# Kernel tuning notes

Hardware: AMD Instinct MI355X
Metric: run time of the kernel (lower is better)

The kernel has to match this reference:

```python
import jax, jax.numpy as jnp
import numpy as np

N = 100_000      # nodes
E = 1_600_000    # edges (avg degree 16)
D_IN = 128
D_OUT = 128
K = 64           # low-rank attention rank


def setup_inputs() -> dict:
    key = jax.random.key(0)
    ks = jax.random.split(key, 6)
    s = lambda d: 1.0 / np.sqrt(d)
    return {
        "x": jax.random.normal(ks[0], (N, D_IN), dtype=jnp.float32),
        "edge_index": jax.random.randint(ks[1], (2, E), 0, N, dtype=jnp.int32),
        "W_gcn": jax.random.normal(ks[2], (D_IN, D_OUT), dtype=jnp.float32) * s(D_IN),
        "b_gcn": jnp.zeros((D_OUT,), jnp.float32),
        "W_att": jax.random.normal(ks[3], (D_IN, 4 * K), dtype=jnp.float32) * s(D_IN),
        "b_att": jnp.zeros((4 * K,), jnp.float32),
        "W_red": jax.random.normal(ks[4], (D_OUT + 2 * K, D_OUT), dtype=jnp.float32) * s(D_OUT + 2 * K),
        "b_red": jnp.zeros((D_OUT,), jnp.float32),
    }


def _forward(x, W_gcn, b_gcn, W_att, b_att, W_red, b_red, edge_index):
    n = x.shape[0]
    # --- GCN conv (symmetric normalization, self-loops), dropout = identity (eval) ---
    loop = jnp.arange(n, dtype=edge_index.dtype)
    src = jnp.concatenate([edge_index[0], loop])
    dst = jnp.concatenate([edge_index[1], loop])
    deg = jax.ops.segment_sum(jnp.ones_like(dst, dtype=x.dtype), dst, num_segments=n)
    dinv = jax.lax.rsqrt(deg)                      # deg >= 1 due to self-loops
    norm = dinv[src] * dinv[dst]                   # [E+n]
    h = x @ W_gcn                                  # [n, D_OUT]
    agg = jax.ops.segment_sum(h[src] * norm[:, None], dst, num_segments=n) + b_gcn
    x_local = jax.nn.relu(agg)

    # --- Low-rank global attention (LRGA) ---
    t = jax.nn.relu(x @ W_att + b_att)             # [n, 4K]
    U, V, Z, T = jnp.split(t, 4, axis=1)           # each [n, K]
    # joint_normalize2: scalar 1/mean(U @ (V^T @ 1_n))
    D = 1.0 / jnp.mean(U @ (V.T @ jnp.ones((n, 1), x.dtype)))
    res = (U @ (V.T @ Z)) * D                      # [n, K]
    x_global = jnp.concatenate([res, T], axis=1)   # [n, 2K]

    # --- fuse + dim reduce ---
    return jnp.concatenate([x_local, x_global], axis=1) @ W_red + b_red


def reference(x, edge_index, W_gcn, b_gcn, W_att, b_att, W_red, b_red):
    return _forward(x, W_gcn, b_gcn, W_att, b_att, W_red, b_red, edge_index)
```

## Files before the change

### kernel.cpp

```cpp
#include <hip/hip_runtime.h>

#define DIN   128
#define DOUT  128
#define KR    64
#define TCOLS 256
#define WCOLS 384
#define P_RED 512
#define PSTR  4224
#define STCAP 6144

typedef unsigned short ushort_t;
typedef __attribute__((ext_vector_type(8))) short bf16x8;
typedef __attribute__((ext_vector_type(4))) float f32x4;

__device__ __forceinline__ float bf2f(unsigned short u) {
  return __uint_as_float(((unsigned int)u) << 16);
}
__device__ __forceinline__ unsigned short f2bf(float f) {
  unsigned int b = __float_as_uint(f);
  b = b + 0x7FFFu + ((b >> 16) & 1u);
  return (unsigned short)(b >> 16);
}

__global__ __launch_bounds__(256) void k_init(int* __restrict__ degc, float* __restrict__ VtZ,
                                              float* __restrict__ colsum, int* __restrict__ bcur,
                                              int* __restrict__ ocnt, int N) {
  int i = blockIdx.x * 256 + threadIdx.x;
  if (i < N) degc[i] = 1;
  if (i < 4096) VtZ[i] = 0.f;
  if (i < 128) colsum[i] = 0.f;
  if (i < 128) bcur[i] = 0;
  if (i == 0) ocnt[0] = 0;
}

__global__ __launch_bounds__(256) void k_split(const float* __restrict__ x,
                                               ushort_t* __restrict__ xhF, ushort_t* __restrict__ xloF,
                                               int N, int total_slots) {
  int gid = blockIdx.x * 256 + threadIdx.x;
  int stride = gridDim.x * 256;
  for (; gid < total_slots; gid += stride) {
    int f = gid >> 6, l = gid & 63;
    int r16 = f >> 2, s = f & 3;
    int row = r16 * 16 + (l & 15);
    int k = s * 32 + ((l >> 4) << 3);
    ushort4 h0, h1, l0, l1;
    if (row < N) {
      float4 a = *(const float4*)&x[(size_t)row * DIN + k];
      float4 b = *(const float4*)&x[(size_t)row * DIN + k + 4];
      h0.x = f2bf(a.x); h0.y = f2bf(a.y); h0.z = f2bf(a.z); h0.w = f2bf(a.w);
      h1.x = f2bf(b.x); h1.y = f2bf(b.y); h1.z = f2bf(b.z); h1.w = f2bf(b.w);
      l0.x = f2bf(a.x - bf2f(h0.x)); l0.y = f2bf(a.y - bf2f(h0.y));
      l0.z = f2bf(a.z - bf2f(h0.z)); l0.w = f2bf(a.w - bf2f(h0.w));
      l1.x = f2bf(b.x - bf2f(h1.x)); l1.y = f2bf(b.y - bf2f(h1.y));
      l1.z = f2bf(b.z - bf2f(h1.z)); l1.w = f2bf(b.w - bf2f(h1.w));
    } else {
      h0 = make_ushort4(0, 0, 0, 0); h1 = h0; l0 = h0; l1 = h0;
    }
    ((ushort4*)xhF)[gid * 2] = h0;
    ((ushort4*)xhF)[gid * 2 + 1] = h1;
    ((ushort4*)xloF)[gid * 2] = l0;
    ((ushort4*)xloF)[gid * 2 + 1] = l1;
  }
}

__global__ __launch_bounds__(256) void k_wprep(const float* __restrict__ Wg, const float* __restrict__ Wa,
                                               ushort_t* __restrict__ whF, ushort_t* __restrict__ wlF) {
  int g = blockIdx.x * 256 + threadIdx.x;
  int f = g >> 6, l = g & 63;
  int c16 = f >> 2, s = f & 3;
  int col = c16 * 16 + (l & 15);
  int k = s * 32 + ((l >> 4) << 3);
#pragma unroll
  for (int j = 0; j < 8; ++j) {
    float v = (col < DOUT) ? Wg[(size_t)(k + j) * DOUT + col]
                           : Wa[(size_t)(k + j) * TCOLS + (col - DOUT)];
    ushort_t h = f2bf(v);
    whF[(size_t)g * 8 + j] = h;
    wlF[(size_t)g * 8 + j] = f2bf(v - bf2f(h));
  }
}

__global__ __launch_bounds__(256) void k_scan1(const int* __restrict__ degc, int* __restrict__ offs,
                                               int* __restrict__ bsums, int N) {
  __shared__ int s[256];
  int tid = threadIdx.x;
  int base = blockIdx.x * 1024 + tid * 4;
  int c[4], e[4];
#pragma unroll
  for (int q = 0; q < 4; ++q) c[q] = (base + q < N) ? (degc[base + q] - 1) : 0;
  e[0] = 0; e[1] = c[0]; e[2] = e[1] + c[1]; e[3] = e[2] + c[2];
  int tsum = e[3] + c[3];
  s[tid] = tsum; __syncthreads();
  for (int off = 1; off < 256; off <<= 1) {
    int v = (tid >= off) ? s[tid - off] : 0;
    __syncthreads();
    s[tid] += v;
    __syncthreads();
  }
  int tb = s[tid] - tsum;
#pragma unroll
  for (int q = 0; q < 4; ++q) if (base + q < N) offs[base + q] = tb + e[q];
  if (tid == 255) bsums[blockIdx.x] = s[255];
}

__global__ __launch_bounds__(128) void k_scan2(const int* __restrict__ bsums, int* __restrict__ boff,
                                               int* __restrict__ offs, int NBLK, int N) {
  __shared__ int s[128];
  int tid = threadIdx.x;
  int v = (tid < NBLK) ? bsums[tid] : 0;
  s[tid] = v; __syncthreads();
  for (int off = 1; off < 128; off <<= 1) {
    int u = (tid >= off) ? s[tid - off] : 0;
    __syncthreads();
    s[tid] += u;
    __syncthreads();
  }
  boff[tid] = s[tid] - v;
  if (tid == 127) offs[N] = s[127];
}

__global__ __launch_bounds__(256) void k_scan3(int* __restrict__ offs, const int* __restrict__ boff,
                                               const int* __restrict__ degc, float* __restrict__ dinv,
                                               int N) {
  int i = blockIdx.x * 256 + threadIdx.x;
  if (i < N) {
    offs[i] += boff[i >> 10];
    dinv[i] = rsqrtf((float)degc[i]);
  }
}

__global__ __launch_bounds__(256) void k_bin(const int* __restrict__ ei, int* __restrict__ bcur,
                                             int* __restrict__ degc,
                                             int2* __restrict__ buckets,
                                             int2* __restrict__ oflow, int* __restrict__ ocnt,
                                             int E, int B, int CAP) {
  __shared__ int hist[128], pref[128], place[128], gbase[128];
  __shared__ int2 st[4096];
  int tid = threadIdx.x;
  int e0 = blockIdx.x * 4096;
  int nE = min(4096, E - e0);
  if (nE <= 0) return;

  if (tid < 128) { hist[tid] = 0; place[tid] = 0; }
  __syncthreads();

  int src[16], dst[16];
#pragma unroll
  for (int q = 0; q < 16; ++q) {
    int idx = tid + q * 256;
    if (idx < nE) {
      src[q] = ei[e0 + idx];
      dst[q] = ei[E + e0 + idx];
      atomicAdd(&hist[dst[q] >> 10], 1);
      atomicAdd(&degc[dst[q]], 1);
    }
  }
  __syncthreads();

  if (tid < 128) pref[tid] = hist[tid];
  __syncthreads();
  for (int off = 1; off < 128; off <<= 1) {
    int v = (tid < 128 && tid >= off) ? pref[tid - off] : 0;
    __syncthreads();
    if (tid < 128) pref[tid] += v;
    __syncthreads();
  }
  if (tid < 128) pref[tid] -= hist[tid];
  if (tid < B && hist[tid] > 0) gbase[tid] = atomicAdd(&bcur[tid], hist[tid]);
  __syncthreads();

#pragma unroll
  for (int q = 0; q < 16; ++q) {
    int idx = tid + q * 256;
    if (idx < nE) {
      int b = dst[q] >> 10;
      int p = pref[b] + atomicAdd(&place[b], 1);
      st[p] = make_int2(src[q], dst[q]);
    }
  }
  __syncthreads();

  for (int i = tid; i < nE; i += 256) {
    int2 q = st[i];
    int b = q.y >> 10;
    int gp = gbase[b] + (i - pref[b]);
    if (gp < CAP) {
      buckets[(size_t)b * CAP + gp] = q;
    } else {
      int oi = atomicAdd(ocnt, 1);
      oflow[oi] = q;
    }
  }
}

__global__ __launch_bounds__(256) void k_scatter2(const int2* __restrict__ buckets,
                                                  const int* __restrict__ bcur,
                                                  const int* __restrict__ offs,
                                                  const float* __restrict__ dinv,
                                                  const int2* __restrict__ oflow,
                                                  const int* __restrict__ ocnt,
                                                  int2* __restrict__ csr, int CAP, int N) {
  __shared__ int lcur[256];
  __shared__ int2 st[STCAP];
  int cb = blockIdx.x >> 2;
  int lo = cb * 1024 + (blockIdx.x & 3) * 256;
  if (lo >= N) return;
  int tid = threadIdx.x;
  int nnode = min(256, N - lo);
  int base = offs[lo];
  int nb = offs[lo + nnode] - base;
  if (tid < nnode) lcur[tid] = offs[lo + tid];
  __syncthreads();
  int avail = min(bcur[cb], CAP);
  const int2* sp = &buckets[(size_t)cb * CAP];
  bool staged = (nb <= STCAP);
  int quarter = lo >> 8;
  for (int i = tid; i < avail; i += 256) {
    int2 q = sp[i];
    if ((q.y >> 8) != quarter) continue;
    int p = atomicAdd(&lcur[q.y - lo], 1);
    int2 c;
    c.x = q.x;
    c.y = __float_as_int(dinv[q.x] * dinv[q.y]);
    if (staged) st[p - base] = c;
    else        csr[p] = c;
  }
  __syncthreads();
  if (staged) {
    for (int i = tid; i < nb; i += 256) csr[base + i] = st[i];
  }
  __syncthreads();
  int n = ocnt[0];
  for (int i = tid; i < n; i += 256) {
    int2 q = oflow[i];
    if ((q.y >> 8) != quarter) continue;
    int p = atomicAdd(&lcur[q.y - lo], 1);
    int2 c;
    c.x = q.x;
    c.y = __float_as_int(dinv[q.x] * dinv[q.y]);
    csr[p] = c;
  }
}

#define LOADK(S, AH, AL, BH, BL)                                              \
  {                                                                           \
    _Pragma("unroll") for (int m_ = 0; m_ < 4; ++m_) {                        \
      size_t fo_ = (((size_t)(r16b + m_) * 4 + (S)) * 64 + lane) * 8;         \
      AH[m_] = *(const bf16x8*)&xhF[fo_];                                     \
      AL[m_] = *(const bf16x8*)&xloF[fo_];                                    \
    }                                                                         \
    _Pragma("unroll") for (int n_ = 0; n_ < 4; ++n_) {                        \
      size_t fo_ = (((size_t)(c16b + n_) * 4 + (S)) * 64 + lane) * 8;         \
      BH[n_] = *(const bf16x8*)&whF[fo_];                                     \
      BL[n_] = *(const bf16x8*)&wlF[fo_];                                     \
    }                                                                         \
  }

__global__ __launch_bounds__(256) void k_gemm1_mfma(const ushort_t* __restrict__ xhF,
                                                    const ushort_t* __restrict__ xloF,
                                                    const ushort_t* __restrict__ whF,
                                                    const ushort_t* __restrict__ wlF,
                                                    const float* __restrict__ ba,
                                                    ushort_t* __restrict__ hs, ushort_t* __restrict__ t,
                                                    int N, int ntiles) {
  int bid = blockIdx.x;
  int g = bid / 24;
  int rem = bid - g * 24;
  int colblk = rem >> 3;
  int ytile = g * 8 + (rem & 7);
  if (ytile >= ntiles) return;

  int tid = threadIdx.x;
  int lane = tid & 63;
  int wave = tid >> 6;
  int wr = wave >> 1, wc = wave & 1;
  int rowbase = ytile * 128 + wr * 64;
  int gcb = colblk * 128 + wc * 64;
  int r16b = ytile * 8 + wr * 4;
  int c16b = colblk * 8 + wc * 4;
  int lr = lane & 15;
  int rq = (lane >> 4) * 4;

  f32x4 acc[4][4] = {};
  bf16x8 ah[2][4], al[2][4], bh[2][4], bl[2][4];

  LOADK(0, ah[0], al[0], bh[0], bl[0]);
#pragma unroll
  for (int s = 0; s < 4; ++s) {
    int cur = s & 1, nxt = cur ^ 1;
    if (s < 3) LOADK(s + 1, ah[nxt], al[nxt], bh[nxt], bl[nxt]);
#pragma unroll
    for (int m = 0; m < 4; ++m)
#pragma unroll
      for (int n = 0; n < 4; ++n) {
        acc[m][n] = __builtin_amdgcn_mfma_f32_16x16x32_bf16(ah[cur][m], bl[cur][n], acc[m][n], 0, 0, 0);
        acc[m][n] = __builtin_amdgcn_mfma_f32_16x16x32_bf16(al[cur][m], bh[cur][n], acc[m][n], 0, 0, 0);
        acc[m][n] = __builtin_amdgcn_mfma_f32_16x16x32_bf16(ah[cur][m], bh[cur][n], acc[m][n], 0, 0, 0);
      }
  }

  if (colblk == 0) {
#pragma unroll
    for (int m = 0; m < 4; ++m)
#pragma unroll
      for (int i = 0; i < 4; ++i) {
        int row = rowbase + m * 16 + rq + i;
        if (row < N) {
#pragma unroll
          for (int n = 0; n < 4; ++n)
            hs[(size_t)row * DOUT + gcb + n * 16 + lr] = f2bf(acc[m][n][i]);
        }
      }
  } else {
    float bav[4];
#pragma unroll
    for (int n = 0; n < 4; ++n) bav[n] = ba[gcb - DOUT + n * 16 + lr];
#pragma unroll
    for (int m = 0; m < 4; ++m)
#pragma unroll
      for (int i = 0; i < 4; ++i) {
        int row = rowbase + m * 16 + rq + i;
        if (row < N) {
#pragma unroll
          for (int n = 0; n < 4; ++n)
            t[(size_t)row * TCOLS + gcb - DOUT + n * 16 + lr] =
                f2bf(fmaxf(acc[m][n][i] + bav[n], 0.f));
        }
      }
  }
}

#define STAGE_RED(BUF, TILE)                                                     \
  {                                                                              \
    int r0_ = (TILE) * 32;                                                       \
    for (int i_ = tid; i_ < 768; i_ += 256) {                                    \
      int r_ = i_ / 24, c0_ = (i_ % 24) * 8;                                     \
      int row_ = r0_ + r_;                                                       \
      ushort4 v0_, v1_;                                                          \
      if (row_ < N) {                                                            \
        v0_ = ((const ushort4*)&t[(size_t)row_ * TCOLS + c0_])[0];               \
        v1_ = ((const ushort4*)&t[(size_t)row_ * TCOLS + c0_])[1];               \
      } else {                                                                   \
        v0_ = make_ushort4(0, 0, 0, 0); v1_ = v0_;                               \
      }                                                                          \
      *(ushort4*)&ts[BUF][r_ * 200 + c0_] = v0_;                                 \
      *(ushort4*)&ts[BUF][r_ * 200 + c0_ + 4] = v1_;                             \
    }                                                                            \
  }

__global__ __launch_bounds__(256) void k_red(const ushort_t* __restrict__ t, float* __restrict__ part,
                                             int N) {
  __shared__ ushort_t ts[2][32 * 200];
  __shared__ float csh[512];
  int tid = threadIdx.x;
  int lane = tid & 63;
  int w = tid >> 6;
  int lr = lane & 15;
  int lk = (lane >> 4) * 8;
  int vcol = 64 + w * 16 + lr;
  int col2 = lane * 2;

  f32x4 acc[4] = {};
  float cs0 = 0.f, cs1 = 0.f;
  int ntiles = (N + 31) >> 5;
  int cur = 0;

  int tile = blockIdx.x;
  if (tile < ntiles) STAGE_RED(0, tile);
  __syncthreads();
  for (; tile < ntiles; tile += gridDim.x) {
    int nxt = tile + gridDim.x;
    if (nxt < ntiles) STAGE_RED(cur ^ 1, nxt);
    const ushort_t* tb = ts[cur];
    bf16x8 a, b[4];
#pragma unroll
    for (int j = 0; j < 8; ++j)
      ((ushort_t*)&a)[j] = tb[(lk + j) * 200 + vcol];
#pragma unroll
    for (int n = 0; n < 4; ++n)
#pragma unroll
      for (int j = 0; j < 8; ++j)
        ((ushort_t*)&b[n])[j] = tb[(lk + j) * 200 + 128 + n * 16 + lr];
#pragma unroll
    for (int j = 0; j < 8; ++j) {
      ushort2 u = *(const ushort2*)&tb[(w * 8 + j) * 200 + col2];
      cs0 += bf2f(u.x); cs1 += bf2f(u.y);
    }
#pragma unroll
    for (int n = 0; n < 4; ++n)
      acc[n] = __builtin_amdgcn_mfma_f32_16x16x32_bf16(a, b[n], acc[n], 0, 0, 0);
    __syncthreads();
    cur ^= 1;
  }

  float* pb = &part[(size_t)blockIdx.x * PSTR];
  int rq = (lane >> 4) * 4;
#pragma unroll
  for (int n = 0; n < 4; ++n)
#pragma unroll
    for (int i = 0; i < 4; ++i)
      pb[(w * 16 + rq + i) * 64 + n * 16 + lr] = acc[n][i];

  csh[tid] = cs0;
  csh[256 + tid] = cs1;
  __syncthreads();
  if (w == 0) {
    float t0 = csh[lane] + csh[64 + lane] + csh[128 + lane] + csh[192 + lane];
    float t1 = csh[256 + lane] + csh[320 + lane] + csh[384 + lane] + csh[448 + lane];
    pb[4096 + col2] = t0;
    pb[4096 + col2 + 1] = t1;
  }
}

__global__ __launch_bounds__(256) void k_redsum(const float* __restrict__ part,
                                                float* __restrict__ VtZ, float* __restrict__ colsum) {
  __shared__ float s[256];
  int tid = threadIdx.x;
  int j = blockIdx.x * 64 + (tid & 63);
  int bc = tid >> 6;
  float a = 0.f;
#pragma unroll 4
  for (int b = bc; b < P_RED; b += 4) a += part[(size_t)b * PSTR + j];
  s[tid] = a;
  __syncthreads();
  if (bc == 0) {
    float v = s[tid] + s[tid + 64] + s[tid + 128] + s[tid + 192];
    if (j < 4096) VtZ[j] = v;
    else colsum[j - 4096] = v;
  }
}

__global__ __launch_bounds__(256) void k_prep(const float* __restrict__ VtZ,
                                              const float* __restrict__ colsum,
                                              const float* __restrict__ Wr,
                                              ushort_t* __restrict__ weffF, int N) {
  __shared__ float dsh[64];
  __shared__ float Dsh;
  int tid = threadIdx.x;
  if (tid < 64) dsh[tid] = colsum[tid] * colsum[64 + tid];
  __syncthreads();
  if (tid == 0) {
    float p = 0.f;
#pragma unroll 8
    for (int i = 0; i < 64; ++i) p += dsh[i];
    Dsh = (p != 0.f) ? ((float)N / p) : 0.f;
  }
  __syncthreads();
  float Dv = Dsh;

  int g = blockIdx.x * 256 + tid;
  int f = g >> 6, l = g & 63;
  int c16 = f >> 3, s = f & 7;
  int c = c16 * 16 + (l & 15);
  int k0 = s * 32 + ((l >> 4) << 3);
#pragma unroll
  for (int j = 0; j < 8; ++j) {
    int k = k0 + j;
    float v;
    if (k < 128 || k >= 192) {
      v = Wr[(size_t)k * DOUT + c];
    } else {
      int kk = k - 128;
      float acc = 0.f;
      for (int q = 0; q < 64; ++q)
        acc += VtZ[kk * 64 + q] * Wr[(size_t)(128 + q) * DOUT + c];
      v = acc * Dv;
    }
    weffF[(size_t)g * 8 + j] = f2bf(v);
  }
}

__global__ __launch_bounds__(256) void k_aggout(const ushort_t* __restrict__ hs,
                                                const int2* __restrict__ csr,
                                                const int* __restrict__ offs,
                                                const float* __restrict__ dinv,
                                                const float* __restrict__ bg,
                                                const ushort_t* __restrict__ t,
                                                const ushort_t* __restrict__ weffF,
                                                const float* __restrict__ br,
                                                float* __restrict__ out, int N) {
  __shared__ ushort_t ys[32 * 264];
  int tid = threadIdx.x;
  int lane = tid & 63;
  int w = tid >> 6;
  int lr = lane & 15;
  int lk = (lane >> 4) * 8;
  int rq = (lane >> 4) * 4;
  int r0 = blockIdx.x * 32;
  int c2 = 2 * lane;

  for (int i = tid; i < 512; i += 256) {
    int r = i >> 4, c0 = 128 + (i & 15) * 8;
    int row = r0 + r;
    ushort4 v0, v1;
    if (row < N) {
      const ushort_t* src = (c0 < 192) ? &t[(size_t)row * TCOLS + (c0 - 128)]
                                       : &t[(size_t)row * TCOLS + c0];
      v0 = ((const ushort4*)src)[0];
      v1 = ((const ushort4*)src)[1];
    } else {
      v0 = make_ushort4(0, 0, 0, 0); v1 = v0;
    }
    *(ushort4*)&ys[r * 264 + c0] = v0;
    *(ushort4*)&ys[r * 264 + c0 + 4] = v1;
  }

  float bg0 = bg[c2], bg1 = bg[c2 + 1];
  for (int q = 0; q < 8; ++q) {
    int r = w * 8 + q;
    int node = r0 + r;
    ushort2 o = make_ushort2(0, 0);
    if (node < N) {
      float dn = dinv[node];
      ushort2 u = *(const ushort2*)&hs[(size_t)node * DOUT + c2];
      float a0 = dn * dn * bf2f(u.x);
      float a1 = dn * dn * bf2f(u.y);
      int e = offs[node], e1 = offs[node + 1];
      for (; e + 4 <= e1; e += 4) {
        int2 q0 = csr[e], q1 = csr[e + 1], q2 = csr[e + 2], q3 = csr[e + 3];
        ushort2 r0v = *(const ushort2*)&hs[(size_t)q0.x * DOUT + c2];
        ushort2 r1v = *(const ushort2*)&hs[(size_t)q1.x * DOUT + c2];
        ushort2 r2v = *(const ushort2*)&hs[(size_t)q2.x * DOUT + c2];
        ushort2 r3v = *(const ushort2*)&hs[(size_t)q3.x * DOUT + c2];
        float n0 = __int_as_float(q0.y), n1 = __int_as_float(q1.y);
        float n2 = __int_as_float(q2.y), n3 = __int_as_float(q3.y);
        a0 += n0 * bf2f(r0v.x) + n1 * bf2f(r1v.x) + n2 * bf2f(r2v.x) + n3 * bf2f(r3v.x);
        a1 += n0 * bf2f(r0v.y) + n1 * bf2f(r1v.y) + n2 * bf2f(r2v.y) + n3 * bf2f(r3v.y);
      }
      for (; e < e1; ++e) {
        int2 qe = csr[e];
        ushort2 rv = *(const ushort2*)&hs[(size_t)qe.x * DOUT + c2];
        float n0 = __int_as_float(qe.y);
        a0 += n0 * bf2f(rv.x);
        a1 += n0 * bf2f(rv.y);
      }
      o.x = f2bf(fmaxf(a0 + bg0, 0.f));
      o.y = f2bf(fmaxf(a1 + bg1, 0.f));
    }
    *(ushort2*)&ys[r * 264 + c2] = o;
  }
  __syncthreads();

  f32x4 acc[2][2] = {};
#pragma unroll
  for (int s = 0; s < 8; ++s) {
    bf16x8 a[2], b[2];
#pragma unroll
    for (int m = 0; m < 2; ++m)
      a[m] = *(const bf16x8*)&ys[(m * 16 + lr) * 264 + s * 32 + lk];
#pragma unroll
    for (int n = 0; n < 2; ++n) {
      int f = (w * 2 + n) * 8 + s;
      b[n] = *(const bf16x8*)&weffF[((size_t)f * 64 + lane) * 8];
    }
#pragma unroll
    for (int m = 0; m < 2; ++m)
#pragma unroll
      for (int n = 0; n < 2; ++n)
        acc[m][n] = __builtin_amdgcn_mfma_f32_16x16x32_bf16(a[m], b[n], acc[m][n], 0, 0, 0);
  }

  float brv[2];
#pragma unroll
  for (int n = 0; n < 2; ++n) brv[n] = br[w * 32 + n * 16 + lr];
#pragma unroll
  for (int m = 0; m < 2; ++m)
#pragma unroll
    for (int i = 0; i < 4; ++i) {
      int row = r0 + m * 16 + rq + i;
      if (row < N) {
#pragma unroll
        for (int n = 0; n < 2; ++n)
          out[(size_t)row * DOUT + w * 32 + n * 16 + lr] = acc[m][n][i] + brv[n];
      }
    }
}

extern "C" void kernel_launch(void* const* d_in, const int* in_sizes, int n_in,
                              void* d_out, int out_size, void* d_ws, size_t ws_size,
                              hipStream_t stream) {
  const float* x  = (const float*)d_in[0];
  const int* ei   = (const int*)d_in[1];
  const float* Wg = (const float*)d_in[2];
  const float* bg = (const float*)d_in[3];
  const float* Wa = (const float*)d_in[4];
  const float* ba = (const float*)d_in[5];
  const float* Wr = (const float*)d_in[6];
  const float* br = (const float*)d_in[7];
  float* out = (float*)d_out;

  const int N = in_sizes[0] / DIN;
  const int E = in_sizes[1] / 2;

  const int NT128 = (N + 127) / 128;
  const int N16P = NT128 * 8;
  const int NFRAG_A = N16P * 4;
  const int B = (N + 1023) >> 10;
  const int CAP = ((E / (B > 0 ? B : 1)) * 3 / 2 + 255) & ~255;

  char* p = (char*)d_ws;
  auto alloc = [&](size_t bytes) {
    char* r = p;
    p += (bytes + 255) & ~(size_t)255;
    return r;
  };
  float* colsum = (float*)alloc(128 * 4);
  float* VtZ    = (float*)alloc(4096 * 4);
  int*   bsums  = (int*)alloc(1024);
  int*   boff   = (int*)alloc(1024);
  int*   bcur   = (int*)alloc(1024);
  int*   ocnt   = (int*)alloc(256);
  ushort_t* weffF = (ushort_t*)alloc(128 * 256 * 2);
  ushort_t* whF = (ushort_t*)alloc((size_t)24 * 4 * 512 * 2);
  ushort_t* wlF = (ushort_t*)alloc((size_t)24 * 4 * 512 * 2);
  float* part   = (float*)alloc((size_t)P_RED * PSTR * 4);
  int*   degc   = (int*)alloc((size_t)N * 4);
  float* dinv   = (float*)alloc((size_t)N * 4);
  int*   offs   = (int*)alloc((size_t)(N + 1) * 4);
  int2*  csr    = (int2*)alloc((size_t)E * 8);
  int2*  buckets= (int2*)alloc((size_t)B * CAP * 8);
  int2*  oflow  = (int2*)alloc((size_t)E * 8);
  ushort_t* xhF = (ushort_t*)alloc((size_t)NFRAG_A * 512 * 2);
  ushort_t* xloF= (ushort_t*)alloc((size_t)NFRAG_A * 512 * 2);
  ushort_t* hs  = (ushort_t*)alloc((size_t)N * DOUT * 2);
  ushort_t* t   = (ushort_t*)alloc((size_t)N * TCOLS * 2);
  (void)ws_size; (void)n_in; (void)out_size;

  const int GN = (N + 255) / 256;
  const int NBLK = (N + 1023) / 1024;
  const int G1 = ((NT128 + 7) / 8) * 24;
  const int GBIN = (E + 4095) / 4096;
  const int NT32 = (N + 31) / 32;

  k_init<<<GN, 256, 0, stream>>>(degc, VtZ, colsum, bcur, ocnt, N);
  k_bin<<<GBIN, 256, 0, stream>>>(ei, bcur, degc, buckets, oflow, ocnt, E, B, CAP);
  k_split<<<2048, 256, 0, stream>>>(x, xhF, xloF, N, NFRAG_A * 64);
  k_wprep<<<24, 256, 0, stream>>>(Wg, Wa, whF, wlF);
  k_scan1<<<NBLK, 256, 0, stream>>>(degc, offs, bsums, N);
  k_scan2<<<1, 128, 0, stream>>>(bsums, boff, offs, NBLK, N);
  k_scan3<<<GN, 256, 0, stream>>>(offs, boff, degc, dinv, N);
  k_scatter2<<<B * 4, 256, 0, stream>>>(buckets, bcur, offs, dinv, oflow, ocnt, csr, CAP, N);
  k_gemm1_mfma<<<G1, 256, 0, stream>>>(xhF, xloF, whF, wlF, ba, hs, t, N, NT128);
  k_red<<<P_RED, 256, 0, stream>>>(t, part, N);
  k_redsum<<<PSTR / 64, 256, 0, stream>>>(part, VtZ, colsum);
  k_prep<<<16, 256, 0, stream>>>(VtZ, colsum, Wr, weffF, N);
  k_aggout<<<NT32, 256, 0, stream>>>(hs, csr, offs, dinv, bg, t, weffF, br, out, N);
}
```

Measured before the change: 418.7 us.

## Fuse x bf16 hi/lo split into GEMM1 via shared-memory staging

Drops the separate k_split kernel, which wrote hi/lo bf16 fragment copies of x to global memory. The GEMM now loads fp32 x directly, splits it into hi/lo parts in shared memory, and uses 64-row tiles with 6 waves covering all 384 output columns, so each x row is read once. This removes a kernel launch and a large round trip through global memory. In exchange there is no register double-buffering, B fragments are reloaded from global by every block, and the blocks are smaller with more shared memory per block.

```diff
diff --git a/kernel.cpp b/kernel.cpp
--- a/kernel.cpp
+++ b/kernel.cpp
@@ -31,36 +31,6 @@
   if (i < 128) colsum[i] = 0.f;
   if (i < 128) bcur[i] = 0;
   if (i == 0) ocnt[0] = 0;
-}
-
-__global__ __launch_bounds__(256) void k_split(const float* __restrict__ x,
-                                               ushort_t* __restrict__ xhF, ushort_t* __restrict__ xloF,
-                                               int N, int total_slots) {
-  int gid = blockIdx.x * 256 + threadIdx.x;
-  int stride = gridDim.x * 256;
-  for (; gid < total_slots; gid += stride) {
-    int f = gid >> 6, l = gid & 63;
-    int r16 = f >> 2, s = f & 3;
-    int row = r16 * 16 + (l & 15);
-    int k = s * 32 + ((l >> 4) << 3);
-    ushort4 h0, h1, l0, l1;
-    if (row < N) {
-      float4 a = *(const float4*)&x[(size_t)row * DIN + k];
-      float4 b = *(const float4*)&x[(size_t)row * DIN + k + 4];
-      h0.x = f2bf(a.x); h0.y = f2bf(a.y); h0.z = f2bf(a.z); h0.w = f2bf(a.w);
-      h1.x = f2bf(b.x); h1.y = f2bf(b.y); h1.z = f2bf(b.z); h1.w = f2bf(b.w);
-      l0.x = f2bf(a.x - bf2f(h0.x)); l0.y = f2bf(a.y - bf2f(h0.y));
-      l0.z = f2bf(a.z - bf2f(h0.z)); l0.w = f2bf(a.w - bf2f(h0.w));
-      l1.x = f2bf(b.x - bf2f(h1.x)); l1.y = f2bf(b.y - bf2f(h1.y));
-      l1.z = f2bf(b.z - bf2f(h1.z)); l1.w = f2bf(b.w - bf2f(h1.w));
-    } else {
-      h0 = make_ushort4(0, 0, 0, 0); h1 = h0; l0 = h0; l1 = h0;
-    }
-    ((ushort4*)xhF)[gid * 2] = h0;
-    ((ushort4*)xhF)[gid * 2 + 1] = h1;
-    ((ushort4*)xloF)[gid * 2] = l0;
-    ((ushort4*)xloF)[gid * 2 + 1] = l1;
-  }
 }
 
 __global__ __launch_bounds__(256) void k_wprep(const float* __restrict__ Wg, const float* __restrict__ Wa,
@@ -242,69 +212,73 @@
   }
 }
 
-#define LOADK(S, AH, AL, BH, BL)                                              \
-  {                                                                           \
-    _Pragma("unroll") for (int m_ = 0; m_ < 4; ++m_) {                        \
-      size_t fo_ = (((size_t)(r16b + m_) * 4 + (S)) * 64 + lane) * 8;         \
-      AH[m_] = *(const bf16x8*)&xhF[fo_];                                     \
-      AL[m_] = *(const bf16x8*)&xloF[fo_];                                    \
-    }                                                                         \
-    _Pragma("unroll") for (int n_ = 0; n_ < 4; ++n_) {                        \
-      size_t fo_ = (((size_t)(c16b + n_) * 4 + (S)) * 64 + lane) * 8;         \
-      BH[n_] = *(const bf16x8*)&whF[fo_];                                     \
-      BL[n_] = *(const bf16x8*)&wlF[fo_];                                     \
-    }                                                                         \
-  }
-
-__global__ __launch_bounds__(256) void k_gemm1_mfma(const ushort_t* __restrict__ xhF,
-                                                    const ushort_t* __restrict__ xloF,
-                                                    const ushort_t* __restrict__ whF,
-                                                    const ushort_t* __restrict__ wlF,
-                                                    const float* __restrict__ ba,
-                                                    ushort_t* __restrict__ hs, ushort_t* __restrict__ t,
-                                                    int N, int ntiles) {
-  int bid = blockIdx.x;
-  int g = bid / 24;
-  int rem = bid - g * 24;
-  int colblk = rem >> 3;
-  int ytile = g * 8 + (rem & 7);
-  if (ytile >= ntiles) return;
-
+__global__ __launch_bounds__(384) void k_gemm1f(const float* __restrict__ x,
+                                                const ushort_t* __restrict__ whF,
+                                                const ushort_t* __restrict__ wlF,
+                                                const float* __restrict__ ba,
+                                                ushort_t* __restrict__ hs, ushort_t* __restrict__ t,
+                                                int N) {
+  __shared__ ushort_t ahs[16 * 512];
+  __shared__ ushort_t als[16 * 512];
   int tid = threadIdx.x;
   int lane = tid & 63;
-  int wave = tid >> 6;
-  int wr = wave >> 1, wc = wave & 1;
-  int rowbase = ytile * 128 + wr * 64;
-  int gcb = colblk * 128 + wc * 64;
-  int r16b = ytile * 8 + wr * 4;
-  int c16b = colblk * 8 + wc * 4;
+  int w = tid >> 6;
+  int r0 = blockIdx.x * 64;
+
+  for (int idx = tid; idx < 2048; idx += 384) {
+    int r = idx >> 5;
+    int k = (idx & 31) * 4;
+    int row = r0 + r;
+    float4 v = (row < N) ? *(const float4*)&x[(size_t)row * DIN + k]
+                         : make_float4(0.f, 0.f, 0.f, 0.f);
+    ushort4 h, l;
+    h.x = f2bf(v.x); h.y = f2bf(v.y); h.z = f2bf(v.z); h.w = f2bf(v.w);
+    l.x = f2bf(v.x - bf2f(h.x)); l.y = f2bf(v.y - bf2f(h.y));
+    l.z = f2bf(v.z - bf2f(h.z)); l.w = f2bf(v.w - bf2f(h.w));
+    int frag = (r >> 4) * 4 + (k >> 5);
+    int slot = (r & 15) + (((k & 31) >> 3) << 4);
+    int off = frag * 512 + slot * 8 + (k & 7);
+    *(ushort4*)&ahs[off] = h;
+    *(ushort4*)&als[off] = l;
+  }
+  __syncthreads();
+
   int lr = lane & 15;
   int rq = (lane >> 4) * 4;
-
+  int c16b = w * 4;
   f32x4 acc[4][4] = {};
-  bf16x8 ah[2][4], al[2][4], bh[2][4], bl[2][4];
-
-  LOADK(0, ah[0], al[0], bh[0], bl[0]);
+
 #pragma unroll
   for (int s = 0; s < 4; ++s) {
-    int cur = s & 1, nxt = cur ^ 1;
-    if (s < 3) LOADK(s + 1, ah[nxt], al[nxt], bh[nxt], bl[nxt]);
+    bf16x8 ahf[4], alf[4], bhf[4], blf[4];
+#pragma unroll
+    for (int m = 0; m < 4; ++m) {
+      ahf[m] = *(const bf16x8*)&ahs[(m * 4 + s) * 512 + lane * 8];
+      alf[m] = *(const bf16x8*)&als[(m * 4 + s) * 512 + lane * 8];
+    }
+#pragma unroll
+    for (int n = 0; n < 4; ++n) {
+      size_t fo = (((size_t)(c16b + n) * 4 + s) * 64 + lane) * 8;
+      bhf[n] = *(const bf16x8*)&whF[fo];
+      blf[n] = *(const bf16x8*)&wlF[fo];
+    }
 #pragma unroll
     for (int m = 0; m < 4; ++m)
 #pragma unroll
       for (int n = 0; n < 4; ++n) {
-        acc[m][n] = __builtin_amdgcn_mfma_f32_16x16x32_bf16(ah[cur][m], bl[cur][n], acc[m][n], 0, 0, 0);
-        acc[m][n] = __builtin_amdgcn_mfma_f32_16x16x32_bf16(al[cur][m], bh[cur][n], acc[m][n], 0, 0, 0);
-        acc[m][n] = __builtin_amdgcn_mfma_f32_16x16x32_bf16(ah[cur][m], bh[cur][n], acc[m][n], 0, 0, 0);
+        acc[m][n] = __builtin_amdgcn_mfma_f32_16x16x32_bf16(ahf[m], blf[n], acc[m][n], 0, 0, 0);
+        acc[m][n] = __builtin_amdgcn_mfma_f32_16x16x32_bf16(alf[m], bhf[n], acc[m][n], 0, 0, 0);
+        acc[m][n] = __builtin_amdgcn_mfma_f32_16x16x32_bf16(ahf[m], bhf[n], acc[m][n], 0, 0, 0);
       }
   }
 
-  if (colblk == 0) {
+  int gcb = w * 64;
+  if (w < 2) {
 #pragma unroll
     for (int m = 0; m < 4; ++m)
 #pragma unroll
       for (int i = 0; i < 4; ++i) {
-        int row = rowbase + m * 16 + rq + i;
+        int row = r0 + m * 16 + rq + i;
         if (row < N) {
 #pragma unroll
           for (int n = 0; n < 4; ++n)
@@ -312,18 +286,19 @@
         }
       }
   } else {
+    int cb = gcb - 128;
     float bav[4];
 #pragma unroll
-    for (int n = 0; n < 4; ++n) bav[n] = ba[gcb - DOUT + n * 16 + lr];
+    for (int n = 0; n < 4; ++n) bav[n] = ba[cb + n * 16 + lr];
 #pragma unroll
     for (int m = 0; m < 4; ++m)
 #pragma unroll
       for (int i = 0; i < 4; ++i) {
-        int row = rowbase + m * 16 + rq + i;
+        int row = r0 + m * 16 + rq + i;
         if (row < N) {
 #pragma unroll
           for (int n = 0; n < 4; ++n)
-            t[(size_t)row * TCOLS + gcb - DOUT + n * 16 + lr] =
+            t[(size_t)row * TCOLS + cb + n * 16 + lr] =
                 f2bf(fmaxf(acc[m][n][i] + bav[n], 0.f));
         }
       }
@@ -592,9 +567,6 @@
   const int N = in_sizes[0] / DIN;
   const int E = in_sizes[1] / 2;
 
-  const int NT128 = (N + 127) / 128;
-  const int N16P = NT128 * 8;
-  const int NFRAG_A = N16P * 4;
   const int B = (N + 1023) >> 10;
   const int CAP = ((E / (B > 0 ? B : 1)) * 3 / 2 + 255) & ~255;
 
@@ -620,27 +592,24 @@
   int2*  csr    = (int2*)alloc((size_t)E * 8);
   int2*  buckets= (int2*)alloc((size_t)B * CAP * 8);
   int2*  oflow  = (int2*)alloc((size_t)E * 8);
-  ushort_t* xhF = (ushort_t*)alloc((size_t)NFRAG_A * 512 * 2);
-  ushort_t* xloF= (ushort_t*)alloc((size_t)NFRAG_A * 512 * 2);
   ushort_t* hs  = (ushort_t*)alloc((size_t)N * DOUT * 2);
   ushort_t* t   = (ushort_t*)alloc((size_t)N * TCOLS * 2);
   (void)ws_size; (void)n_in; (void)out_size;
 
   const int GN = (N + 255) / 256;
   const int NBLK = (N + 1023) / 1024;
-  const int G1 = ((NT128 + 7) / 8) * 24;
   const int GBIN = (E + 4095) / 4096;
+  const int NT64 = (N + 63) / 64;
   const int NT32 = (N + 31) / 32;
 
   k_init<<<GN, 256, 0, stream>>>(degc, VtZ, colsum, bcur, ocnt, N);
   k_bin<<<GBIN, 256, 0, stream>>>(ei, bcur, degc, buckets, oflow, ocnt, E, B, CAP);
-  k_split<<<2048, 256, 0, stream>>>(x, xhF, xloF, N, NFRAG_A * 64);
   k_wprep<<<24, 256, 0, stream>>>(Wg, Wa, whF, wlF);
   k_scan1<<<NBLK, 256, 0, stream>>>(degc, offs, bsums, N);
   k_scan2<<<1, 128, 0, stream>>>(bsums, boff, offs, NBLK, N);
   k_scan3<<<GN, 256, 0, stream>>>(offs, boff, degc, dinv, N);
   k_scatter2<<<B * 4, 256, 0, stream>>>(buckets, bcur, offs, dinv, oflow, ocnt, csr, CAP, N);
-  k_gemm1_mfma<<<G1, 256, 0, stream>>>(xhF, xloF, whF, wlF, ba, hs, t, N, NT128);
+  k_gemm1f<<<NT64, 384, 0, stream>>>(x, whF, wlF, ba, hs, t, N);
   k_red<<<P_RED, 256, 0, stream>>>(t, part, N);
   k_redsum<<<PSTR / 64, 256, 0, stream>>>(part, VtZ, colsum);
   k_prep<<<16, 256, 0, stream>>>(VtZ, colsum, Wr, weffF, N);
```

Measured after the change: 424.7 us. No clear change (+1.4%).
